# Performance work log

Hardware: AMD Instinct MI355X
Metric: run time of the kernel (lower is better)

The kernel has to match this reference:

```python
import jax, jax.numpy as jnp
import numpy as np

GROUPS = 32
EPS = 1e-5
HEADS = 8
HEAD_DIM = 40
INNER = HEADS * HEAD_DIM  # 320
QUERY_DIM = 320
CONTEXT_DIM = 768


def setup_inputs() -> dict:
    key = jax.random.key(0)
    ks = jax.random.split(key, 9)
    B, C, H, W = 16, QUERY_DIM, 64, 64
    Lc = 77
    x = jax.random.normal(ks[0], (B, C, H, W), dtype=jnp.float32)
    context = jax.random.normal(ks[1], (B, Lc, CONTEXT_DIM), dtype=jnp.float32)
    # Linear weights in torch layout (out_features, in_features), no bias for q/k/v
    Wq = jax.random.normal(ks[2], (INNER, QUERY_DIM), dtype=jnp.float32) * (QUERY_DIM ** -0.5)
    Wk = jax.random.normal(ks[3], (INNER, CONTEXT_DIM), dtype=jnp.float32) * (CONTEXT_DIM ** -0.5)
    Wv = jax.random.normal(ks[4], (INNER, CONTEXT_DIM), dtype=jnp.float32) * (CONTEXT_DIM ** -0.5)
    Wo = jax.random.normal(ks[5], (QUERY_DIM, INNER), dtype=jnp.float32) * (INNER ** -0.5)
    bo = jnp.zeros((QUERY_DIM,), dtype=jnp.float32)
    gn_scale = jnp.ones((QUERY_DIM,), dtype=jnp.float32)
    gn_bias = jnp.zeros((QUERY_DIM,), dtype=jnp.float32)
    return {"x": x, "context": context, "Wq": Wq, "Wk": Wk, "Wv": Wv,
            "Wo": Wo, "bo": bo, "gn_scale": gn_scale, "gn_bias": gn_bias}


def _group_norm(x, scale, bias):
    # x: [B, C, H, W]
    B, C, H, W = x.shape
    xg = x.reshape(B, GROUPS, C // GROUPS, H, W)
    mean = jnp.mean(xg, axis=(2, 3, 4), keepdims=True)
    var = jnp.var(xg, axis=(2, 3, 4), keepdims=True)
    xn = ((xg - mean) * jax.lax.rsqrt(var + EPS)).reshape(B, C, H, W)
    return xn * scale[None, :, None, None] + bias[None, :, None, None]


def reference(x, context, Wq, Wk, Wv, Wo, bo, gn_scale, gn_bias):
    B, C, H, W = x.shape
    residual = x
    xn = _group_norm(x, gn_scale, gn_bias)
    # (B, C, H, W) -> (B, H*W, C)
    tokens = xn.reshape(B, C, H * W).transpose(0, 2, 1)
    S = H * W
    Lc = context.shape[1]
    scale = HEAD_DIM ** -0.5
    # projections (Linear: x @ W.T); split heads -> [B, h, S, d]
    q = jnp.einsum('bsc,ec->bse', tokens, Wq).reshape(B, S, HEADS, HEAD_DIM).transpose(0, 2, 1, 3)
    k = jnp.einsum('blc,ec->ble', context, Wk).reshape(B, Lc, HEADS, HEAD_DIM).transpose(0, 2, 1, 3)
    v = jnp.einsum('blc,ec->ble', context, Wv).reshape(B, Lc, HEADS, HEAD_DIM).transpose(0, 2, 1, 3)
    scores = jnp.einsum('bhsd,bhkd->bhsk', q, k) * scale  # [B, h, S, Lc]
    attn = jax.nn.softmax(scores, axis=-1)
    out = jnp.einsum('bhsk,bhkd->bhsd', attn, v)  # [B, h, S, d]
    out = out.transpose(0, 2, 1, 3).reshape(B, S, INNER)
    out = jnp.einsum('bse,ce->bsc', out, Wo) + bo  # to_out (dropout is identity at eval)
    out = out.transpose(0, 2, 1).reshape(B, C, H, W)
    return out + residual
```

## Files before the change

### kernel.cpp

```cpp
#include <hip/hip_runtime.h>
#include <hip/hip_bf16.h>
#include <stdint.h>

#define B_    16
#define C_    320
#define S_    4096
#define G_    32
#define LC    77
#define CTX   768
#define HEADS 8
#define HD    40

typedef __bf16 bf16x8_t __attribute__((ext_vector_type(8)));
typedef float  f32x4_t  __attribute__((ext_vector_type(4)));

__device__ __forceinline__ unsigned short f2bf(float f) {
    union { float f; unsigned int u; } v; v.f = f;
    unsigned int r = v.u + 0x7fffu + ((v.u >> 16) & 1u);
    return (unsigned short)(r >> 16);
}
__device__ __forceinline__ float bf2f(unsigned short h) {
    union { unsigned int u; float f; } v; v.u = ((unsigned int)h) << 16;
    return v.f;
}

__device__ __forceinline__ void gload16(const void* g, void* l) {
    __builtin_amdgcn_global_load_lds(
        (const __attribute__((address_space(1))) unsigned int*)g,
        (__attribute__((address_space(3))) unsigned int*)l, 16, 0, 0);
}

__global__ __launch_bounds__(256) void gn_stats(const float* __restrict__ x,
                                                float2* __restrict__ mr) {
    int bg = blockIdx.x;
    const float4* p = (const float4*)(x + (size_t)bg * 40960);
    float s = 0.f, s2 = 0.f;
    for (int i = threadIdx.x; i < 10240; i += 256) {
        float4 v = p[i];
        s  += v.x + v.y + v.z + v.w;
        s2 += v.x * v.x + v.y * v.y + v.z * v.z + v.w * v.w;
    }
    for (int o = 32; o; o >>= 1) {
        s  += __shfl_down(s, o);
        s2 += __shfl_down(s2, o);
    }
    __shared__ float2 red[4];
    int lane = threadIdx.x & 63, wid = threadIdx.x >> 6;
    if (lane == 0) red[wid] = make_float2(s, s2);
    __syncthreads();
    if (threadIdx.x == 0) {
        float a = 0.f, c = 0.f;
        for (int i = 0; i < 4; i++) { a += red[i].x; c += red[i].y; }
        float mean = a / 40960.f;
        float var  = c / 40960.f - mean * mean;
        mr[bg] = make_float2(mean, rsqrtf(var + 1e-5f));
    }
}

__global__ __launch_bounds__(256) void castw(const float* __restrict__ s,
                                             unsigned short* __restrict__ d) {
    int i = blockIdx.x * 256 + threadIdx.x;
    float4 v = ((const float4*)s)[i];
    ushort4 o;
    o.x = f2bf(v.x); o.y = f2bf(v.y); o.z = f2bf(v.z); o.w = f2bf(v.w);
    ((ushort4*)d)[i] = o;
}

__global__ __launch_bounds__(256) void norm_tr(const float* __restrict__ x,
                                               const float2* __restrict__ mr,
                                               const float* __restrict__ gns,
                                               const float* __restrict__ gnb,
                                               unsigned short* __restrict__ tok) {
    int s0 = blockIdx.x * 32, c0 = blockIdx.y * 32, b = blockIdx.z;
    __shared__ unsigned short t[32][33];
    int tx = threadIdx.x & 31, ty = threadIdx.x >> 5;
    #pragma unroll
    for (int i = 0; i < 4; i++) {
        int cl = i * 8 + ty;
        int c = c0 + cl;
        float2 m = mr[b * 32 + c / 10];
        float v = x[((size_t)(b * 320 + c)) * 4096 + s0 + tx];
        v = (v - m.x) * m.y * gns[c] + gnb[c];
        t[cl][tx] = f2bf(v);
    }
    __syncthreads();
    #pragma unroll
    for (int i = 0; i < 4; i++) {
        int sl = i * 8 + ty;
        tok[((size_t)b * 4096 + s0 + sl) * 320 + c0 + tx] = t[tx][sl];
    }
}

__global__ __launch_bounds__(256) void ukern(const float* __restrict__ Wk,
                                             const float* __restrict__ Wq,
                                             unsigned short* __restrict__ Ut) {
    int c = blockIdx.x, h = blockIdx.y;
    int t = threadIdx.x;
    float a0 = 0.f, a1 = 0.f, a2 = 0.f;
    for (int d = 0; d < HD; d++) {
        float wq = Wq[(size_t)(h * HD + d) * 320 + c];
        const float* wkr = Wk + (size_t)(h * HD + d) * CTX;
        a0 += wq * wkr[t];
        a1 += wq * wkr[t + 256];
        a2 += wq * wkr[t + 512];
    }
    unsigned short* o = Ut + ((size_t)h * 320 + c) * CTX;
    o[t]       = f2bf(a0);
    o[t + 256] = f2bf(a1);
    o[t + 512] = f2bf(a2);
}

__global__ __launch_bounds__(256) void kvM_gemm(const float* __restrict__ ctx,
                                                const float* __restrict__ Wv,
                                                const unsigned short* __restrict__ Ut,
                                                unsigned short* __restrict__ vout,
                                                unsigned short* __restrict__ Mout) {
    __shared__ unsigned short la[64][32], lb[64][32];
    int bm = blockIdx.x, bn = blockIdx.y;
    int tid = threadIdx.x, lane = tid & 63, wid = tid >> 6;
    int wm = wid >> 1, wn = wid & 1;
    int lr = tid >> 2, lc = (tid & 3) * 8;
    int fr = lane & 15, kk = (lane >> 4) * 8;

    int arow = bm * 64 + lr; if (arow > 1231) arow = 1231;
    const float* ap = ctx + (size_t)arow * CTX;
    bool isV = (bn < 5);
    const float* wp = isV ? (Wv + (size_t)(bn * 64 + lr) * CTX) : nullptr;
    const unsigned short* up = isV ? nullptr
        : (Ut + ((size_t)((bn - 5) / 5) * 320 + (size_t)((bn - 5) % 5) * 64 + lr) * CTX);

    f32x4_t acc[2][2] = {};
    for (int k0 = 0; k0 < CTX; k0 += 32) {
        float4 a4 = *(const float4*)&ap[k0 + lc];
        float4 a5 = *(const float4*)&ap[k0 + lc + 4];
        ushort4 pa0 = { f2bf(a4.x), f2bf(a4.y), f2bf(a4.z), f2bf(a4.w) };
        ushort4 pa1 = { f2bf(a5.x), f2bf(a5.y), f2bf(a5.z), f2bf(a5.w) };
        *(ushort4*)&la[lr][lc]     = pa0;
        *(ushort4*)&la[lr][lc + 4] = pa1;
        if (isV) {
            float4 w4 = *(const float4*)&wp[k0 + lc];
            float4 w5 = *(const float4*)&wp[k0 + lc + 4];
            ushort4 pw0 = { f2bf(w4.x), f2bf(w4.y), f2bf(w4.z), f2bf(w4.w) };
            ushort4 pw1 = { f2bf(w5.x), f2bf(w5.y), f2bf(w5.z), f2bf(w5.w) };
            *(ushort4*)&lb[lr][lc]     = pw0;
            *(ushort4*)&lb[lr][lc + 4] = pw1;
        } else {
            *(uint4*)&lb[lr][lc] = *(const uint4*)&up[k0 + lc];
        }
        __syncthreads();
        bf16x8_t a0 = *(const bf16x8_t*)&la[wm * 32 + fr][kk];
        bf16x8_t a1 = *(const bf16x8_t*)&la[wm * 32 + 16 + fr][kk];
        bf16x8_t b0 = *(const bf16x8_t*)&lb[wn * 32 + fr][kk];
        bf16x8_t b1 = *(const bf16x8_t*)&lb[wn * 32 + 16 + fr][kk];
        acc[0][0] = __builtin_amdgcn_mfma_f32_16x16x32_bf16(a0, b0, acc[0][0], 0, 0, 0);
        acc[0][1] = __builtin_amdgcn_mfma_f32_16x16x32_bf16(a0, b1, acc[0][1], 0, 0, 0);
        acc[1][0] = __builtin_amdgcn_mfma_f32_16x16x32_bf16(a1, b0, acc[1][0], 0, 0, 0);
        acc[1][1] = __builtin_amdgcn_mfma_f32_16x16x32_bf16(a1, b1, acc[1][1], 0, 0, 0);
        __syncthreads();
    }
    int rg = (lane >> 4) * 4;
    #pragma unroll
    for (int mf = 0; mf < 2; mf++)
        #pragma unroll
        for (int nf = 0; nf < 2; nf++)
            #pragma unroll
            for (int r = 0; r < 4; r++) {
                int row = bm * 64 + wm * 32 + mf * 16 + rg + r;
                if (row < 1232) {
                    int coloff = wn * 32 + nf * 16 + fr;
                    unsigned short val = f2bf(acc[mf][nf][r]);
                    if (isV) {
                        vout[(size_t)row * 320 + bn * 64 + coloff] = val;
                    } else {
                        int bb = row / 77, kv = row - bb * 77;
                        int hh = (bn - 5) / 5;
                        int c = ((bn - 5) % 5) * 64 + coloff;
                        size_t tile = ((size_t)bb * 8 + hh) * 25600;
                        int idx16 = kv * 40 + (c >> 3);
                        int swz = idx16 ^ (kv & 7);
                        Mout[tile + (size_t)swz * 8 + (c & 7)] = val;
                    }
                }
            }
}

__global__ __launch_bounds__(256, 2) void attn6(const unsigned short* __restrict__ tok,
                                                const unsigned short* __restrict__ M,
                                                const unsigned short* __restrict__ v,
                                                unsigned short* __restrict__ att) {
    __shared__ unsigned short Msr[25600];
    unsigned short (*Ps)[104] = (unsigned short (*)[104])Msr;
    unsigned short (*Vt)[104] = (unsigned short (*)[104])(Msr + 13312);

    int tid = threadIdx.x;
    int qt = blockIdx.x, b = blockIdx.y, h0 = blockIdx.z * 4;
    int q0 = qt * 128;
    int lane = tid & 63, wv = tid >> 6;
    int fr = lane & 15, fg = lane >> 4;
    const float scale = 0.15811388300841898f;

    {
        const unsigned short* Mt = M + ((size_t)b * 8 + h0) * 25600;
        #pragma unroll
        for (int i = 0; i < 13; i++) {
            int u = i * 256 + tid;
            if (u < 3200) gload16(Mt + (size_t)u * 8, &Msr[u * 8]);
        }
    }
    uint4 vreg0, vreg1;
    {
        int r = tid / 5, sg = tid % 5;
        vreg0 = *(const uint4*)&v[((size_t)(b * LC + r)) * 320 + h0 * HD + sg * 8];
        int idx = tid + 256;
        if (idx < 385) {
            r = idx / 5; sg = idx % 5;
            vreg1 = *(const uint4*)&v[((size_t)(b * LC + r)) * 320 + h0 * HD + sg * 8];
        }
    }
    bf16x8_t atok[2][10];
    const size_t tokbase = ((size_t)b * S_ + q0) * 320;
    #pragma unroll
    for (int mf = 0; mf < 2; mf++)
        #pragma unroll
        for (int k = 0; k < 10; k++)
            atok[mf][k] = *(const bf16x8_t*)&tok[tokbase + (size_t)(wv * 32 + mf * 16 + fr) * 320 + k * 32 + fg * 8];

    __syncthreads();

    for (int i = 0; i < 4; i++) {
        int h = h0 + i;

        f32x4_t sc[2][5] = {};
        #pragma unroll
        for (int k = 0; k < 10; k++) {
            bf16x8_t bb[5];
            #pragma unroll
            for (int nf = 0; nf < 5; nf++) {
                int idx16 = (nf * 16 + fr) * 40 + k * 4 + fg;
                bb[nf] = *(const bf16x8_t*)&Msr[(size_t)(idx16 ^ (fr & 7)) * 8];
            }
            #pragma unroll
            for (int mf = 0; mf < 2; mf++)
                #pragma unroll
                for (int nf = 0; nf < 5; nf++)
                    sc[mf][nf] = __builtin_amdgcn_mfma_f32_16x16x32_bf16(atok[mf][k], bb[nf], sc[mf][nf], 0, 0, 0);
        }
        __syncthreads();

        {
            unsigned short e[8];
            int r = tid / 5, sg = tid % 5;
            *(uint4*)e = vreg0;
            #pragma unroll
            for (int j = 0; j < 8; j++) Vt[sg * 8 + j][r] = e[j];
            int idx = tid + 256;
            if (idx < 385) {
                r = idx / 5; sg = idx % 5;
                *(uint4*)e = vreg1;
                #pragma unroll
                for (int j = 0; j < 8; j++) Vt[sg * 8 + j][r] = e[j];
            }
        }

        {
            uint4 z = {0, 0, 0, 0};
            int zr = wv * 32 + (lane >> 1);
            *(uint4*)((char*)&Ps[zr][80] + (lane & 1) * 16) = z;
        }

        float sm[2][4];
        #pragma unroll
        for (int mf = 0; mf < 2; mf++)
            #pragma unroll
            for (int r = 0; r < 4; r++) {
                float s = 0.f;
                #pragma unroll
                for (int nf = 0; nf < 5; nf++) {
                    float p = (nf < 4 || fr < 13) ? __expf(sc[mf][nf][r] * scale) : 0.f;
                    sc[mf][nf][r] = p;
                    s += p;
                }
                sm[mf][r] = s;
            }
        #pragma unroll
        for (int off = 1; off < 16; off <<= 1)
            #pragma unroll
            for (int mf = 0; mf < 2; mf++)
                #pragma unroll
                for (int r = 0; r < 4; r++)
                    sm[mf][r] += __shfl_xor(sm[mf][r], off);

        #pragma unroll
        for (int mf = 0; mf < 2; mf++)
            #pragma unroll
            for (int nf = 0; nf < 5; nf++)
                #pragma unroll
                for (int r = 0; r < 4; r++)
                    Ps[wv * 32 + mf * 16 + fg * 4 + r][nf * 16 + fr] = f2bf(sc[mf][nf][r]);

        __syncthreads();

        f32x4_t ov[2][3] = {};
        #pragma unroll
        for (int ks = 0; ks < 3; ks++) {
            bf16x8_t vb[3];
            #pragma unroll
            for (int nf = 0; nf < 3; nf++)
                vb[nf] = *(const bf16x8_t*)&Vt[nf * 16 + fr][ks * 32 + fg * 8];
            #pragma unroll
            for (int mf = 0; mf < 2; mf++) {
                bf16x8_t pa = *(const bf16x8_t*)&Ps[wv * 32 + mf * 16 + fr][ks * 32 + fg * 8];
                #pragma unroll
                for (int nf = 0; nf < 3; nf++)
                    ov[mf][nf] = __builtin_amdgcn_mfma_f32_16x16x32_bf16(pa, vb[nf], ov[mf][nf], 0, 0, 0);
            }
        }
        __syncthreads();

        if (i < 3) {
            const unsigned short* Mn = M + ((size_t)b * 8 + h + 1) * 25600;
            #pragma unroll
            for (int j = 0; j < 13; j++) {
                int u = j * 256 + tid;
                if (u < 3200) gload16(Mn + (size_t)u * 8, &Msr[u * 8]);
            }
            int r = tid / 5, sg = tid % 5;
            vreg0 = *(const uint4*)&v[((size_t)(b * LC + r)) * 320 + (h + 1) * HD + sg * 8];
            int idx = tid + 256;
            if (idx < 385) {
                r = idx / 5; sg = idx % 5;
                vreg1 = *(const uint4*)&v[((size_t)(b * LC + r)) * 320 + (h + 1) * HD + sg * 8];
            }
        }

        #pragma unroll
        for (int mf = 0; mf < 2; mf++) {
            float inv[4];
            #pragma unroll
            for (int r = 0; r < 4; r++) inv[r] = 1.f / sm[mf][r];
            #pragma unroll
            for (int nf = 0; nf < 3; nf++) {
                int d = nf * 16 + fr;
                if (d < HD) {
                    #pragma unroll
                    for (int r = 0; r < 4; r++) {
                        int qrow = q0 + wv * 32 + mf * 16 + fg * 4 + r;
                        att[((size_t)(b * 8 + h) * S_ + qrow) * 40 + d] = f2bf(ov[mf][nf][r] * inv[r]);
                    }
                }
            }
        }
        if (i < 3) __syncthreads();
    }
}

__global__ __launch_bounds__(256) void gemm_oproj2(const unsigned short* __restrict__ att,
                                                   const unsigned short* __restrict__ wo,
                                                   const float* __restrict__ bo,
                                                   const float* __restrict__ resid,
                                                   float* __restrict__ out) {
    __shared__ unsigned short lw[320 * 40];
    __shared__ unsigned short la[64 * 40];
    int tid = threadIdx.x, lane = tid & 63, wv = tid >> 6;
    int fr = lane & 15, fg = lane >> 4;
    int bm = blockIdx.x, b = blockIdx.y;
    int s0 = bm * 64;

    f32x4_t acc[5][4] = {};

    for (int k0 = 0; k0 < 320; k0 += 32) {
        #pragma unroll
        for (int i = 0; i < 7; i++) {
            int u = i * 256 + tid;
            if (u < 1600) {
                int row = u / 5, ch = u % 5;
                int c = ch < 4 ? ch : 0;
                gload16(wo + (size_t)row * 320 + k0 + c * 8, &lw[(size_t)u * 8]);
            }
        }
        {
            int u = tid;
            int row = u / 5, ch = u % 5;
            int c = ch < 4 ? ch : 0;
            int e0 = k0 + c * 8;
            gload16(att + ((size_t)(b * 8 + e0 / 40) * S_ + s0 + row) * 40 + e0 % 40,
                    &la[(size_t)u * 8]);
            u = tid + 256;
            if (u < 320) {
                row = u / 5; ch = u % 5; c = ch < 4 ? ch : 0;
                e0 = k0 + c * 8;
                gload16(att + ((size_t)(b * 8 + e0 / 40) * S_ + s0 + row) * 40 + e0 % 40,
                        &la[(size_t)u * 8]);
            }
        }
        __syncthreads();
        bf16x8_t bfrag[4];
        #pragma unroll
        for (int sf = 0; sf < 4; sf++)
            bfrag[sf] = *(const bf16x8_t*)&la[(sf * 16 + fr) * 40 + fg * 8];
        #pragma unroll
        for (int nf = 0; nf < 5; nf++) {
            bf16x8_t afrag = *(const bf16x8_t*)&lw[(wv * 80 + nf * 16 + fr) * 40 + fg * 8];
            #pragma unroll
            for (int sf = 0; sf < 4; sf++)
                acc[nf][sf] = __builtin_amdgcn_mfma_f32_16x16x32_bf16(afrag, bfrag[sf], acc[nf][sf], 0, 0, 0);
        }
        __syncthreads();
    }

    int nbase = wv * 80;
    #pragma unroll
    for (int nf = 0; nf < 5; nf++) {
        #pragma unroll
        for (int r = 0; r < 4; r++) {
            int n = nbase + nf * 16 + fg * 4 + r;
            float bov = bo[n];
            size_t rowb = ((size_t)(b * 320 + n)) * 4096 + s0;
            #pragma unroll
            for (int sf = 0; sf < 4; sf++) {
                int s = sf * 16 + fr;
                out[rowb + s] = acc[nf][sf][r] + bov + resid[rowb + s];
            }
        }
    }
}

extern "C" void kernel_launch(void* const* d_in, const int* in_sizes, int n_in,
                              void* d_out, int out_size, void* d_ws, size_t ws_size,
                              hipStream_t stream) {
    const float* x    = (const float*)d_in[0];
    const float* ctx  = (const float*)d_in[1];
    const float* Wq   = (const float*)d_in[2];
    const float* Wk   = (const float*)d_in[3];
    const float* Wv   = (const float*)d_in[4];
    const float* Wo   = (const float*)d_in[5];
    const float* bo   = (const float*)d_in[6];
    const float* gns  = (const float*)d_in[7];
    const float* gnb  = (const float*)d_in[8];
    float* out = (float*)d_out;

    char* ws = (char*)d_ws;
    float2*         mr    = (float2*)(ws + 0);
    unsigned short* wo_bf = (unsigned short*)(ws + 4096);
    unsigned short* v_bf  = (unsigned short*)(ws + 208896);
    unsigned short* Mbuf  = (unsigned short*)(ws + 997376);
    unsigned short* tok   = (unsigned short*)(ws + 7550976);
    unsigned short* att   = (unsigned short*)(ws + 49494016);
    unsigned short* Ut    = att;

    gn_stats<<<512, 256, 0, stream>>>(x, mr);
    castw<<<100, 256, 0, stream>>>(Wo, wo_bf);
    ukern<<<dim3(320, 8), 256, 0, stream>>>(Wk, Wq, Ut);
    kvM_gemm<<<dim3(20, 45), 256, 0, stream>>>(ctx, Wv, Ut, v_bf, Mbuf);
    norm_tr<<<dim3(128, 10, 16), 256, 0, stream>>>(x, mr, gns, gnb, tok);
    attn6<<<dim3(32, 16, 2), 256, 0, stream>>>(tok, Mbuf, v_bf, att);
    gemm_oproj2<<<dim3(64, 16), 256, 0, stream>>>(att, wo_bf, bo, x, out);
}
```

Before: 183.0 us.

## Stage whole attention tile in swizzled LDS and read Wo directly from global

The output-projection kernel now loads the full 64x320 attention tile into LDS once, using an XOR swizzle to avoid bank conflicts. It then reads Wo fragments directly from global/L2 instead of staging Wo per k-step, which removes the per-iteration LDS staging and the barriers inside the k loop. Separately, the V staging in the attention kernel remaps threads so that consecutive threads handle consecutive kv rows, which changes the global load and LDS transpose-write patterns. The risk is the global-load latency on Wo inside the MFMA loop, and the larger LDS footprint, which may reduce occupancy.

```diff
diff --git a/kernel.cpp b/kernel.cpp
--- a/kernel.cpp
+++ b/kernel.cpp
@@ -209,12 +209,12 @@
     }
     uint4 vreg0, vreg1;
     {
-        int r = tid / 5, sg = tid % 5;
-        vreg0 = *(const uint4*)&v[((size_t)(b * LC + r)) * 320 + h0 * HD + sg * 8];
+        int kv = tid % 77, sg = tid / 77;
+        vreg0 = *(const uint4*)&v[((size_t)(b * LC + kv)) * 320 + h0 * HD + sg * 8];
         int idx = tid + 256;
         if (idx < 385) {
-            r = idx / 5; sg = idx % 5;
-            vreg1 = *(const uint4*)&v[((size_t)(b * LC + r)) * 320 + h0 * HD + sg * 8];
+            kv = idx % 77; sg = idx / 77;
+            vreg1 = *(const uint4*)&v[((size_t)(b * LC + kv)) * 320 + h0 * HD + sg * 8];
         }
     }
     bf16x8_t atok[2][10];
@@ -249,16 +249,16 @@
 
         {
             unsigned short e[8];
-            int r = tid / 5, sg = tid % 5;
+            int kv = tid % 77, sg = tid / 77;
             *(uint4*)e = vreg0;
             #pragma unroll
-            for (int j = 0; j < 8; j++) Vt[sg * 8 + j][r] = e[j];
+            for (int j = 0; j < 8; j++) Vt[sg * 8 + j][kv] = e[j];
             int idx = tid + 256;
             if (idx < 385) {
-                r = idx / 5; sg = idx % 5;
+                kv = idx % 77; sg = idx / 77;
                 *(uint4*)e = vreg1;
                 #pragma unroll
-                for (int j = 0; j < 8; j++) Vt[sg * 8 + j][r] = e[j];
+                for (int j = 0; j < 8; j++) Vt[sg * 8 + j][kv] = e[j];
             }
         }
 
@@ -324,12 +324,12 @@
                 int u = j * 256 + tid;
                 if (u < 3200) gload16(Mn + (size_t)u * 8, &Msr[u * 8]);
             }
-            int r = tid / 5, sg = tid % 5;
-            vreg0 = *(const uint4*)&v[((size_t)(b * LC + r)) * 320 + (h + 1) * HD + sg * 8];
+            int kv = tid % 77, sg = tid / 77;
+            vreg0 = *(const uint4*)&v[((size_t)(b * LC + kv)) * 320 + (h + 1) * HD + sg * 8];
             int idx = tid + 256;
             if (idx < 385) {
-                r = idx / 5; sg = idx % 5;
-                vreg1 = *(const uint4*)&v[((size_t)(b * LC + r)) * 320 + (h + 1) * HD + sg * 8];
+                kv = idx % 77; sg = idx / 77;
+                vreg1 = *(const uint4*)&v[((size_t)(b * LC + kv)) * 320 + (h + 1) * HD + sg * 8];
             }
         }
 
@@ -354,58 +354,44 @@
     }
 }
 
-__global__ __launch_bounds__(256) void gemm_oproj2(const unsigned short* __restrict__ att,
+__global__ __launch_bounds__(256) void gemm_oproj3(const unsigned short* __restrict__ att,
                                                    const unsigned short* __restrict__ wo,
                                                    const float* __restrict__ bo,
                                                    const float* __restrict__ resid,
                                                    float* __restrict__ out) {
-    __shared__ unsigned short lw[320 * 40];
-    __shared__ unsigned short la[64 * 40];
+    __shared__ unsigned short la[64 * 320];
     int tid = threadIdx.x, lane = tid & 63, wv = tid >> 6;
     int fr = lane & 15, fg = lane >> 4;
     int bm = blockIdx.x, b = blockIdx.y;
     int s0 = bm * 64;
 
+    #pragma unroll
+    for (int i = 0; i < 10; i++) {
+        int u = i * 256 + tid;
+        int row = u / 40, ch = u % 40;
+        int chs = ch ^ (row & 7);
+        int h = chs / 5, d0 = (chs % 5) * 8;
+        gload16(att + ((size_t)(b * 8 + h) * S_ + s0 + row) * 40 + d0, &la[(size_t)u * 8]);
+    }
+    __syncthreads();
+
     f32x4_t acc[5][4] = {};
-
+    const unsigned short* wop = wo + (size_t)(wv * 80 + fr) * 320 + fg * 8;
     for (int k0 = 0; k0 < 320; k0 += 32) {
-        #pragma unroll
-        for (int i = 0; i < 7; i++) {
-            int u = i * 256 + tid;
-            if (u < 1600) {
-                int row = u / 5, ch = u % 5;
-                int c = ch < 4 ? ch : 0;
-                gload16(wo + (size_t)row * 320 + k0 + c * 8, &lw[(size_t)u * 8]);
-            }
-        }
-        {
-            int u = tid;
-            int row = u / 5, ch = u % 5;
-            int c = ch < 4 ? ch : 0;
-            int e0 = k0 + c * 8;
-            gload16(att + ((size_t)(b * 8 + e0 / 40) * S_ + s0 + row) * 40 + e0 % 40,
-                    &la[(size_t)u * 8]);
-            u = tid + 256;
-            if (u < 320) {
-                row = u / 5; ch = u % 5; c = ch < 4 ? ch : 0;
-                e0 = k0 + c * 8;
-                gload16(att + ((size_t)(b * 8 + e0 / 40) * S_ + s0 + row) * 40 + e0 % 40,
-                        &la[(size_t)u * 8]);
-            }
-        }
-        __syncthreads();
         bf16x8_t bfrag[4];
         #pragma unroll
-        for (int sf = 0; sf < 4; sf++)
-            bfrag[sf] = *(const bf16x8_t*)&la[(sf * 16 + fr) * 40 + fg * 8];
+        for (int sf = 0; sf < 4; sf++) {
+            int row = sf * 16 + fr;
+            int chs = (k0 / 8 + fg) ^ (row & 7);
+            bfrag[sf] = *(const bf16x8_t*)&la[(size_t)(row * 40 + chs) * 8];
+        }
         #pragma unroll
         for (int nf = 0; nf < 5; nf++) {
-            bf16x8_t afrag = *(const bf16x8_t*)&lw[(wv * 80 + nf * 16 + fr) * 40 + fg * 8];
+            bf16x8_t afrag = *(const bf16x8_t*)&wop[(size_t)(nf * 16) * 320 + k0];
             #pragma unroll
             for (int sf = 0; sf < 4; sf++)
                 acc[nf][sf] = __builtin_amdgcn_mfma_f32_16x16x32_bf16(afrag, bfrag[sf], acc[nf][sf], 0, 0, 0);
         }
-        __syncthreads();
     }
 
     int nbase = wv * 80;
@@ -454,5 +440,5 @@
     kvM_gemm<<<dim3(20, 45), 256, 0, stream>>>(ctx, Wv, Ut, v_bf, Mbuf);
     norm_tr<<<dim3(128, 10, 16), 256, 0, stream>>>(x, mr, gns, gnb, tok);
     attn6<<<dim3(32, 16, 2), 256, 0, stream>>>(tok, Mbuf, v_bf, att);
-    gemm_oproj2<<<dim3(64, 16), 256, 0, stream>>>(att, wo_bf, bo, x, out);
-}
+    gemm_oproj3<<<dim3(64, 16), 256, 0, stream>>>(att, wo_bf, bo, x, out);
+}
```

Result: slower. 222.5 us (+21.6%).
